# Kernel tuning notes

Measured on AMD Instinct MI355X. Metric: run time of the kernel, lower is better.

Reference implementation:

```python
import jax, jax.numpy as jnp
import numpy as np

MERSENNE_P = (1 << 31) - 1  # prime used by universal hashing


def _uhash_cols(random_numbers, n_full_cols, n_comp_cols):
    """Universal-hash map from full-weight column index -> compressed column index.
    h(j) = ((r0*j + r1) mod P) mod n_comp_cols  (ints stay well within int64).
    """
    j = jnp.arange(n_full_cols, dtype=jnp.int64)
    r0 = random_numbers[0]
    r1 = random_numbers[1]
    return ((r0 * j + r1) % MERSENNE_P) % n_comp_cols


def setup_inputs() -> dict:
    key = jax.random.key(0)
    k1, k2, k3 = jax.random.split(key, 3)
    in_features, out_features, redn_factor = 8192, 8192, 4
    init_scale = 1.0 / np.sqrt(in_features)
    x = jax.random.normal(k1, (64, in_features), dtype=jnp.float32)
    weight = jax.random.uniform(
        k2, (out_features, in_features // redn_factor), dtype=jnp.float32,
        minval=-init_scale, maxval=init_scale)
    random_numbers = jax.random.randint(k3, (4,), 1, 1048576, dtype=jnp.int64)
    return {"x": x, "weight": weight, "random_numbers": random_numbers,
            "redn_factor": 4}


def reference(x, weight, random_numbers, redn_factor):
    # x: [..., K]; weight (compressed): [N, K // redn_factor]
    orig_shape = x.shape
    K = orig_shape[-1]
    x2d = x.reshape(-1, K)                      # preprocess: flatten leading dims
    n_comp = weight.shape[1]
    col_idx = _uhash_cols(random_numbers, K, n_comp)   # [K] hashed gather indices
    w_full = weight[:, col_idx]                 # [N, K] expanded via hashed gather
    y = x2d @ w_full.T                          # [rows, N]
    return y.reshape(*orig_shape[:-1], y.shape[-1])  # postprocess
```

## Files before the change

### kernel.cpp

```cpp
#include <hip/hip_runtime.h>
#include <hip/hip_bf16.h>

#define K_FULL   8192
#define M_ROWS   64
#define N_OUT    8192
#define N_COMP   2048
#define P_MERS   2147483647


typedef __attribute__((ext_vector_type(8))) short bf16x8;
typedef __attribute__((ext_vector_type(4))) float f32x4;

__device__ __forceinline__ short f2bfs(float f) {
    __hip_bfloat16 h = __float2bfloat16(f);
    return *reinterpret_cast<short*>(&h);
}

__device__ __forceinline__ int hash_col(int j, int rn0, int rn1, int rn2, int rn3) {
    if (rn1 == 0 && rn3 == 0) {
        unsigned long long xx = (unsigned long long)(unsigned int)rn0 * (unsigned int)j
                              + (unsigned long long)(unsigned int)rn2;
        unsigned long long t = (xx & (unsigned long long)P_MERS) + (xx >> 31);
        if (t >= (unsigned long long)P_MERS) t -= (unsigned long long)P_MERS;
        return (int)(t & (N_COMP - 1));
    } else {
        unsigned int t = (unsigned int)rn0 * (unsigned int)j + (unsigned int)rn1;
        int ti = (int)t;
        int m1 = ti % P_MERS;
        if (m1 < 0) m1 += P_MERS;
        return m1 & (N_COMP - 1);
    }
}

__global__ __launch_bounds__(1024) void k_xc(const float* __restrict__ x,
                                             const int* __restrict__ rn,
                                             unsigned int* __restrict__ xcF) {
    __shared__ float row[N_COMP];
    const int m = blockIdx.x;
    const int tid = threadIdx.x;
    row[tid] = 0.0f;
    row[tid + 1024] = 0.0f;
    const int rn0 = rn[0], rn1 = rn[1], rn2 = rn[2], rn3 = rn[3];
    __syncthreads();

    const float* xm = x + (size_t)m * K_FULL;
#pragma unroll
    for (int it = 0; it < 2; ++it) {
        int j0 = tid * 4 + it * 4096;
        float4 v = *(const float4*)(xm + j0);
        atomicAdd(&row[hash_col(j0 + 0, rn0, rn1, rn2, rn3)], v.x);
        atomicAdd(&row[hash_col(j0 + 1, rn0, rn1, rn2, rn3)], v.y);
        atomicAdd(&row[hash_col(j0 + 2, rn0, rn1, rn2, rn3)], v.z);
        atomicAdd(&row[hash_col(j0 + 3, rn0, rn1, rn2, rn3)], v.w);
    }
    __syncthreads();

    const int c0 = 2 * tid;
    const int s  = c0 >> 5;
    const int kg = (c0 >> 3) & 3;
    const int e0 = c0 & 7;
    const int g  = m >> 4;
    const int nr = m & 15;
    unsigned int pk = (unsigned int)(unsigned short)f2bfs(row[c0])
                    | ((unsigned int)(unsigned short)f2bfs(row[c0 + 1]) << 16);
    xcF[(((s * 4 + g) * 64 + kg * 16 + nr) << 2) + (e0 >> 1)] = pk;
}

__global__ __launch_bounds__(512) void k_gemm(const float* __restrict__ W,
                                              const unsigned short* __restrict__ xcF,
                                              float* __restrict__ y) {
    __shared__ float ys[8][M_ROWS][16];
    const int tid  = threadIdx.x;
    const int lane = tid & 63;
    const int w    = __builtin_amdgcn_readfirstlane(tid >> 6);
    const int nr   = lane & 15;
    const int kg   = lane >> 4;
    const int n0   = blockIdx.x * 16;

    const float* wp = W + (size_t)(n0 + nr) * N_COMP + w * 32 + kg * 8;
    const unsigned short* ap = xcF + (size_t)w * 2048 + lane * 8;

    f32x4 acc0 = {0.f, 0.f, 0.f, 0.f};
    f32x4 acc1 = {0.f, 0.f, 0.f, 0.f};
    f32x4 acc2 = {0.f, 0.f, 0.f, 0.f};
    f32x4 acc3 = {0.f, 0.f, 0.f, 0.f};

#define LOADW(W0, W1, T) do { int o_ = (T) * 256;                      \
        (W0) = *(const float4*)(wp + o_);                              \
        (W1) = *(const float4*)(wp + o_ + 4); } while (0)
#define LOADA(A0, A1, A2, A3, T) do {                                  \
        const unsigned short* p_ = ap + (size_t)(T) * 16384;           \
        (A0) = *(const bf16x8*)(p_);                                   \
        (A1) = *(const bf16x8*)(p_ + 512);                             \
        (A2) = *(const bf16x8*)(p_ + 1024);                            \
        (A3) = *(const bf16x8*)(p_ + 1536); } while (0)
#define DOMFMA(W0, W1, A0, A1, A2, A3) do { bf16x8 b_;                 \
        b_[0] = f2bfs((W0).x); b_[1] = f2bfs((W0).y);                  \
        b_[2] = f2bfs((W0).z); b_[3] = f2bfs((W0).w);                  \
        b_[4] = f2bfs((W1).x); b_[5] = f2bfs((W1).y);                  \
        b_[6] = f2bfs((W1).z); b_[7] = f2bfs((W1).w);                  \
        acc0 = __builtin_amdgcn_mfma_f32_16x16x32_bf16((A0), b_, acc0, 0, 0, 0); \
        acc1 = __builtin_amdgcn_mfma_f32_16x16x32_bf16((A1), b_, acc1, 0, 0, 0); \
        acc2 = __builtin_amdgcn_mfma_f32_16x16x32_bf16((A2), b_, acc2, 0, 0, 0); \
        acc3 = __builtin_amdgcn_mfma_f32_16x16x32_bf16((A3), b_, acc3, 0, 0, 0); } while (0)

    float4 wa0, wa1, wb0, wb1;
    bf16x8 aa0, aa1, aa2, aa3, ab0, ab1, ab2, ab3;

    LOADW(wa0, wa1, 0);
    LOADA(aa0, aa1, aa2, aa3, 0);
#pragma unroll 1
    for (int t = 0; t < 6; t += 2) {
        LOADW(wb0, wb1, t + 1);
        LOADA(ab0, ab1, ab2, ab3, t + 1);
        DOMFMA(wa0, wa1, aa0, aa1, aa2, aa3);
        LOADW(wa0, wa1, t + 2);
        LOADA(aa0, aa1, aa2, aa3, t + 2);
        DOMFMA(wb0, wb1, ab0, ab1, ab2, ab3);
    }
    LOADW(wb0, wb1, 7);
    LOADA(ab0, ab1, ab2, ab3, 7);
    DOMFMA(wa0, wa1, aa0, aa1, aa2, aa3);
    DOMFMA(wb0, wb1, ab0, ab1, ab2, ab3);

#pragma unroll
    for (int j = 0; j < 4; ++j) {
        ys[w][ 0 + kg * 4 + j][nr] = acc0[j];
        ys[w][16 + kg * 4 + j][nr] = acc1[j];
        ys[w][32 + kg * 4 + j][nr] = acc2[j];
        ys[w][48 + kg * 4 + j][nr] = acc3[j];
    }
    __syncthreads();

#pragma unroll
    for (int i = 0; i < 2; ++i) {
        int o = tid + 512 * i;
        int m = o >> 4;
        int n = o & 15;
        float s = 0.f;
#pragma unroll
        for (int q = 0; q < 8; ++q) s += ys[q][m][n];
        y[(size_t)m * N_OUT + n0 + n] = s;
    }
}

extern "C" void kernel_launch(void* const* d_in, const int* in_sizes, int n_in,
                              void* d_out, int out_size, void* d_ws, size_t ws_size,
                              hipStream_t stream) {
    const float* x = (const float*)d_in[0];
    const float* W = (const float*)d_in[1];
    const int* rn  = (const int*)d_in[2];
    float* y       = (float*)d_out;

    unsigned int* xcF = (unsigned int*)d_ws;

    k_xc<<<M_ROWS, 1024, 0, stream>>>(x, rn, xcF);
    k_gemm<<<N_OUT / 16, 512, 0, stream>>>(W, (const unsigned short*)xcF, y);
}
```

Baseline: 34.30 us.

## Give each wave a contiguous K slab with per-block rotated start order

```diff
diff --git a/kernel.cpp b/kernel.cpp
--- a/kernel.cpp
+++ b/kernel.cpp
@@ -14,6 +14,10 @@
 __device__ __forceinline__ short f2bfs(float f) {
     __hip_bfloat16 h = __float2bfloat16(f);
     return *reinterpret_cast<short*>(&h);
+}
+__device__ __forceinline__ unsigned int pk2bf(float a, float b) {
+    return (unsigned int)(unsigned short)f2bfs(a)
+         | ((unsigned int)(unsigned short)f2bfs(b) << 16);
 }
 
 __device__ __forceinline__ int hash_col(int j, int rn0, int rn1, int rn2, int rn3) {
@@ -61,67 +65,50 @@
     const int e0 = c0 & 7;
     const int g  = m >> 4;
     const int nr = m & 15;
-    unsigned int pk = (unsigned int)(unsigned short)f2bfs(row[c0])
-                    | ((unsigned int)(unsigned short)f2bfs(row[c0 + 1]) << 16);
-    xcF[(((s * 4 + g) * 64 + kg * 16 + nr) << 2) + (e0 >> 1)] = pk;
+    xcF[(((s * 4 + g) * 64 + kg * 16 + nr) << 2) + (e0 >> 1)] =
+        pk2bf(row[c0], row[c0 + 1]);
 }
 
-__global__ __launch_bounds__(512) void k_gemm(const float* __restrict__ W,
+__global__ __launch_bounds__(256) void k_gemm(const float* __restrict__ W,
                                               const unsigned short* __restrict__ xcF,
                                               float* __restrict__ y) {
-    __shared__ float ys[8][M_ROWS][16];
+    __shared__ float ys[4][M_ROWS][16];
     const int tid  = threadIdx.x;
     const int lane = tid & 63;
     const int w    = __builtin_amdgcn_readfirstlane(tid >> 6);
     const int nr   = lane & 15;
     const int kg   = lane >> 4;
     const int n0   = blockIdx.x * 16;
+    const int rot  = blockIdx.x & 15;
 
-    const float* wp = W + (size_t)(n0 + nr) * N_COMP + w * 32 + kg * 8;
-    const unsigned short* ap = xcF + (size_t)w * 2048 + lane * 8;
+    const float* wp = W + (size_t)(n0 + nr) * N_COMP + w * 512 + kg * 8;
+    const unsigned short* ab = xcF + (size_t)w * 16 * 2048 + lane * 8;
 
     f32x4 acc0 = {0.f, 0.f, 0.f, 0.f};
     f32x4 acc1 = {0.f, 0.f, 0.f, 0.f};
     f32x4 acc2 = {0.f, 0.f, 0.f, 0.f};
     f32x4 acc3 = {0.f, 0.f, 0.f, 0.f};
 
-#define LOADW(W0, W1, T) do { int o_ = (T) * 256;                      \
-        (W0) = *(const float4*)(wp + o_);                              \
-        (W1) = *(const float4*)(wp + o_ + 4); } while (0)
-#define LOADA(A0, A1, A2, A3, T) do {                                  \
-        const unsigned short* p_ = ap + (size_t)(T) * 16384;           \
-        (A0) = *(const bf16x8*)(p_);                                   \
-        (A1) = *(const bf16x8*)(p_ + 512);                             \
-        (A2) = *(const bf16x8*)(p_ + 1024);                            \
-        (A3) = *(const bf16x8*)(p_ + 1536); } while (0)
-#define DOMFMA(W0, W1, A0, A1, A2, A3) do { bf16x8 b_;                 \
-        b_[0] = f2bfs((W0).x); b_[1] = f2bfs((W0).y);                  \
-        b_[2] = f2bfs((W0).z); b_[3] = f2bfs((W0).w);                  \
-        b_[4] = f2bfs((W1).x); b_[5] = f2bfs((W1).y);                  \
-        b_[6] = f2bfs((W1).z); b_[7] = f2bfs((W1).w);                  \
-        acc0 = __builtin_amdgcn_mfma_f32_16x16x32_bf16((A0), b_, acc0, 0, 0, 0); \
-        acc1 = __builtin_amdgcn_mfma_f32_16x16x32_bf16((A1), b_, acc1, 0, 0, 0); \
-        acc2 = __builtin_amdgcn_mfma_f32_16x16x32_bf16((A2), b_, acc2, 0, 0, 0); \
-        acc3 = __builtin_amdgcn_mfma_f32_16x16x32_bf16((A3), b_, acc3, 0, 0, 0); } while (0)
-
-    float4 wa0, wa1, wb0, wb1;
-    bf16x8 aa0, aa1, aa2, aa3, ab0, ab1, ab2, ab3;
-
-    LOADW(wa0, wa1, 0);
-    LOADA(aa0, aa1, aa2, aa3, 0);
-#pragma unroll 1
-    for (int t = 0; t < 6; t += 2) {
-        LOADW(wb0, wb1, t + 1);
-        LOADA(ab0, ab1, ab2, ab3, t + 1);
-        DOMFMA(wa0, wa1, aa0, aa1, aa2, aa3);
-        LOADW(wa0, wa1, t + 2);
-        LOADA(aa0, aa1, aa2, aa3, t + 2);
-        DOMFMA(wb0, wb1, ab0, ab1, ab2, ab3);
+#pragma unroll
+    for (int s = 0; s < 16; ++s) {
+        const int sk = (s + rot) & 15;
+        float4 w0 = *(const float4*)(wp + sk * 32);
+        float4 w1 = *(const float4*)(wp + sk * 32 + 4);
+        const unsigned short* ap = ab + (size_t)sk * 2048;
+        bf16x8 a0 = *(const bf16x8*)(ap);
+        bf16x8 a1 = *(const bf16x8*)(ap + 512);
+        bf16x8 a2 = *(const bf16x8*)(ap + 1024);
+        bf16x8 a3 = *(const bf16x8*)(ap + 1536);
+        bf16x8 b;
+        b[0] = f2bfs(w0.x); b[1] = f2bfs(w0.y);
+        b[2] = f2bfs(w0.z); b[3] = f2bfs(w0.w);
+        b[4] = f2bfs(w1.x); b[5] = f2bfs(w1.y);
+        b[6] = f2bfs(w1.z); b[7] = f2bfs(w1.w);
+        acc0 = __builtin_amdgcn_mfma_f32_16x16x32_bf16(a0, b, acc0, 0, 0, 0);
+        acc1 = __builtin_amdgcn_mfma_f32_16x16x32_bf16(a1, b, acc1, 0, 0, 0);
+        acc2 = __builtin_amdgcn_mfma_f32_16x16x32_bf16(a2, b, acc2, 0, 0, 0);
+        acc3 = __builtin_amdgcn_mfma_f32_16x16x32_bf16(a3, b, acc3, 0, 0, 0);
     }
-    LOADW(wb0, wb1, 7);
-    LOADA(ab0, ab1, ab2, ab3, 7);
-    DOMFMA(wa0, wa1, aa0, aa1, aa2, aa3);
-    DOMFMA(wb0, wb1, ab0, ab1, ab2, ab3);
 
 #pragma unroll
     for (int j = 0; j < 4; ++j) {
@@ -133,13 +120,11 @@
     __syncthreads();
 
 #pragma unroll
-    for (int i = 0; i < 2; ++i) {
-        int o = tid + 512 * i;
+    for (int i = 0; i < 4; ++i) {
+        int o = tid + 256 * i;
         int m = o >> 4;
         int n = o & 15;
-        float s = 0.f;
-#pragma unroll
-        for (int q = 0; q < 8; ++q) s += ys[q][m][n];
+        float s = ys[0][m][n] + ys[1][m][n] + ys[2][m][n] + ys[3][m][n];
         y[(size_t)m * N_OUT + n0 + n] = s;
     }
 }
@@ -155,5 +140,5 @@
     unsigned int* xcF = (unsigned int*)d_ws;
 
     k_xc<<<M_ROWS, 1024, 0, stream>>>(x, rn, xcF);
-    k_gemm<<<N_OUT / 16, 512, 0, stream>>>(W, (const unsigned short*)xcF, y);
+    k_gemm<<<N_OUT / 16, 256, 0, stream>>>(W, (const unsigned short*)xcF, y);
 }
```

After: 31.24 us. 8.9% less time.
